# Performance work log

Measured on AMD Instinct MI355X. Metric: run time of the kernel, lower is better.

## Reference

```python
import jax, jax.numpy as jnp
import numpy as np

MAX_SPAN_WIDTH = 30
NUM_WORDS = 2048
NUM_CAND = 8192
HIDDEN = 768
FEAT = 20
FFNN = 1000
SPAN_DIM = HIDDEN * 3 + FEAT  # 2324
TOP_SPAN_NUM = int(NUM_WORDS * 0.4)  # 819


def setup_inputs() -> dict:
    key = jax.random.key(0)
    ks = jax.random.split(key, 16)
    mention_doc = jax.random.normal(ks[0], (NUM_WORDS, HIDDEN), jnp.float32)
    starts = jax.random.randint(ks[1], (NUM_CAND,), 0, NUM_WORDS - MAX_SPAN_WIDTH, jnp.int32)
    widths = jax.random.randint(ks[2], (NUM_CAND,), 1, MAX_SPAN_WIDTH + 1, jnp.int32)
    ends = jnp.minimum(starts + widths - 1, NUM_WORDS - 1).astype(jnp.int32)
    s = 0.02
    lin = lambda k, i, o: jax.random.normal(k, (i, o), jnp.float32) * s
    return dict(
        mention_doc=mention_doc,
        span_width_emb=jax.random.normal(ks[3], (MAX_SPAN_WIDTH, FEAT), jnp.float32) * s,
        head_w=jax.random.normal(ks[4], (HIDDEN,), jnp.float32) * s,
        head_b=jnp.zeros((), jnp.float32),
        m_w1=lin(ks[5], SPAN_DIM, FFNN), m_b1=jnp.zeros((FFNN,), jnp.float32),
        m_w2=lin(ks[6], FFNN, FFNN), m_b2=jnp.zeros((FFNN,), jnp.float32),
        m_w3=jax.random.normal(ks[7], (FFNN,), jnp.float32) * s, m_b3=jnp.zeros((), jnp.float32),
        width_prior_emb=jax.random.normal(ks[8], (MAX_SPAN_WIDTH, FEAT), jnp.float32) * s,
        w_w1=lin(ks[9], FEAT, FFNN), w_b1=jnp.zeros((FFNN,), jnp.float32),
        w_w2=lin(ks[10], FFNN, FFNN), w_b2=jnp.zeros((FFNN,), jnp.float32),
        w_w3=jax.random.normal(ks[11], (FFNN,), jnp.float32) * s, w_b3=jnp.zeros((), jnp.float32),
        candidate_starts=starts,
        candidate_ends=ends,
        top_span_num=TOP_SPAN_NUM,
    )


def get_span_emb(mention_doc, starts, ends, span_width_emb, head_w, head_b):
    # mention_doc: [N, H]; starts/ends: [C]
    num_words = mention_doc.shape[0]
    start_emb = mention_doc[starts]              # [C, H]
    end_emb = mention_doc[ends]                  # [C, H]
    width_ids = ends - starts                    # span width - 1, in [0, MAX_SPAN_WIDTH)
    width_emb = span_width_emb[width_ids]        # [C, F]
    offs = jnp.arange(MAX_SPAN_WIDTH, dtype=starts.dtype)
    idxes = jnp.minimum(starts[:, None] + offs[None, :], num_words - 1)  # [C, W]
    emb_spans = mention_doc[idxes]               # [C, W, H]  (dominant intermediate)
    head_scores = mention_doc @ head_w + head_b  # [N]
    hs = head_scores[idxes]                      # [C, W]
    mask = offs[None, :] <= width_ids[:, None]
    hs = jnp.where(mask, hs, -jnp.inf)
    attn = jax.nn.softmax(hs, axis=1)            # masked softmax over span positions
    attended = jnp.einsum('cw,cwh->ch', attn, emb_spans)
    return jnp.concatenate([start_emb, end_emb, width_emb, attended], axis=-1)  # [C, 3H+F]


def ffnn3(x, w1, b1, w2, b2, w3, b3):
    h = jax.nn.relu(x @ w1 + b1)
    h = jax.nn.relu(h @ w2 + b2)
    return h @ w3 + b3  # [..., ] scalar score per row (Squeezer)


def extract_top_spans(span_scores, starts, ends, top_span_num, num_words):
    # Greedy crossing-interval NMS, faithful to the original sequential algorithm.
    C = span_scores.shape[0]
    order = jnp.argsort(-span_scores)
    offs = jnp.arange(MAX_SPAN_WIDTH, dtype=jnp.int32)

    def body(i, state):
        max_end, min_start, sel, count = state
        idx = order[i]
        s = starts[idx]
        e = ends[idx]
        dup = max_end[s] == e
        j_raw = s + offs
        j = jnp.minimum(j_raw, num_words - 1)
        in_span = j_raw <= e
        # crossing: an already-selected span starting at j>s ends beyond e,
        # or one ending at j<e starts before s.
        c1 = in_span & (j_raw > s) & (max_end[j] > e)
        c2 = in_span & (j_raw < e) & (min_start[j] < s)
        crossed = jnp.any(c1 | c2)
        accept = (~dup) & (~crossed) & (count < top_span_num)
        sel = jnp.where(accept, sel.at[count].set(idx.astype(jnp.int32)), sel)
        max_end = jnp.where(accept, max_end.at[s].max(e), max_end)
        min_start = jnp.where(accept, min_start.at[e].min(s), min_start)
        count = count + accept.astype(jnp.int32)
        return (max_end, min_start, sel, count)

    max_end0 = jnp.full((num_words,), -1, jnp.int32)          # 'not set' sentinel
    min_start0 = jnp.full((num_words,), num_words, jnp.int32)  # 'not set' sentinel
    sel0 = jnp.zeros((top_span_num,), jnp.int32)
    _, _, sel, count = jax.lax.fori_loop(0, C, body, (max_end0, min_start0, sel0, jnp.int32(0)))

    # sort selected spans by (start, end); pad unfilled slots with the first sorted span
    valid = jnp.arange(top_span_num) < count
    keys = jnp.where(valid, starts[sel] * num_words + ends[sel], jnp.iinfo(jnp.int32).max)
    sorted_sel = sel[jnp.argsort(keys)]
    return jnp.where(valid, sorted_sel, sorted_sel[0])


def reference(mention_doc, span_width_emb, head_w, head_b,
              m_w1, m_b1, m_w2, m_b2, m_w3, m_b3,
              width_prior_emb, w_w1, w_b1, w_w2, w_b2, w_w3, w_b3,
              candidate_starts, candidate_ends, top_span_num):
    num_words = mention_doc.shape[0]
    span_emb = get_span_emb(mention_doc, candidate_starts, candidate_ends,
                            span_width_emb, head_w, head_b)            # [C, 2324]
    mention_scores = ffnn3(span_emb, m_w1, m_b1, m_w2, m_b2, m_w3, m_b3)  # [C]
    width_scores = ffnn3(width_prior_emb, w_w1, w_b1, w_w2, w_b2, w_w3, w_b3)  # [30]
    cand_mention_scores = mention_scores + width_scores[candidate_ends - candidate_starts]
    top_idx = extract_top_spans(cand_mention_scores, candidate_starts, candidate_ends,
                                top_span_num, num_words)               # [top]
    top_starts = candidate_starts[top_idx]
    top_ends = candidate_ends[top_idx]
    top_span_emb = span_emb[top_idx]
    top_scores = cand_mention_scores[top_idx]
    return (cand_mention_scores, top_idx, top_starts, top_ends, top_span_emb, top_scores)
```

## Files before the change

kernel.cpp:

```cpp
#include <hip/hip_runtime.h>
#include <cstdio>
#include <cmath>

#define NUM_WORDS 2048
#define NUM_CAND 8192
#define HIDDEN 768
#define FEAT 20
#define FFNN_DIM 1000
#define SPAN_DIM 2324
#define TOP_NUM 819
#define MSW 30
#define KP2 1024
#define NP 1024
#define PNP 3072

#define OUT_TOPIDX   (NUM_CAND)
#define OUT_TSTART   (NUM_CAND + TOP_NUM)
#define OUT_TEND     (NUM_CAND + 2*TOP_NUM)
#define OUT_TEMB     (NUM_CAND + 3*TOP_NUM)
#define OUT_TSCORE   (NUM_CAND + 3*TOP_NUM + TOP_NUM*SPAN_DIM)

typedef short short8 __attribute__((ext_vector_type(8)));
typedef float f32x4 __attribute__((ext_vector_type(4)));
typedef unsigned short u16x4 __attribute__((ext_vector_type(4)));

__device__ __forceinline__ unsigned short bf16_rne(float x) {
    unsigned int u = __float_as_uint(x);
    unsigned int r = u + 0x7FFFu + ((u >> 16) & 1u);
    return (unsigned short)(r >> 16);
}
__device__ __forceinline__ float bf16_to_f(unsigned short h) {
    return __uint_as_float(((unsigned int)h) << 16);
}
__device__ __forceinline__ void store_split3(unsigned short* p0, unsigned short* p1,
                                             unsigned short* p2, size_t off, float v) {
    unsigned short h0 = bf16_rne(v);
    float r1 = v - bf16_to_f(h0);
    unsigned short h1 = bf16_rne(r1);
    float r2 = r1 - bf16_to_f(h1);
    p0[off] = h0;
    p1[off] = h1;
    p2[off] = bf16_rne(r2);
}

__device__ __forceinline__ void gl_lds16(const unsigned short* g, unsigned short* l) {
    __builtin_amdgcn_global_load_lds(
        (const __attribute__((address_space(1))) unsigned short*)g,
        (__attribute__((address_space(3))) unsigned short*)l, 16, 0, 0);
}

__global__ void head_kernel(const float* __restrict__ doc, const float* __restrict__ hw,
                            const float* __restrict__ hb, float* __restrict__ out) {
    int wave = threadIdx.x >> 6, lane = threadIdx.x & 63;
    int row = blockIdx.x * 4 + wave;
    if (row >= NUM_WORDS) return;
    float acc = 0.f;
    for (int h = lane; h < HIDDEN; h += 64) acc += doc[row * HIDDEN + h] * hw[h];
    for (int off = 32; off > 0; off >>= 1) acc += __shfl_down(acc, off);
    if (lane == 0) out[row] = acc + hb[0];
}

__global__ void width_kernel(const float* __restrict__ x, const float* __restrict__ w1,
                             const float* __restrict__ b1, const float* __restrict__ w2,
                             const float* __restrict__ b2, const float* __restrict__ w3,
                             const float* __restrict__ b3, float* __restrict__ out) {
    __shared__ float xs[FEAT];
    __shared__ float h1s[FFNN_DIM];
    __shared__ float red[256];
    int r = blockIdx.x, t = threadIdx.x;
    if (t < FEAT) xs[t] = x[r * FEAT + t];
    __syncthreads();
    for (int j = t; j < FFNN_DIM; j += 256) {
        float acc = b1[j];
        for (int k = 0; k < FEAT; ++k) acc += xs[k] * w1[k * FFNN_DIM + j];
        h1s[j] = fmaxf(acc, 0.f);
    }
    __syncthreads();
    float partial = 0.f;
    for (int j = t; j < FFNN_DIM; j += 256) {
        float acc = b2[j];
        for (int k = 0; k < FFNN_DIM; ++k) acc += h1s[k] * w2[k * FFNN_DIM + j];
        partial += fmaxf(acc, 0.f) * w3[j];
    }
    red[t] = partial;
    __syncthreads();
    for (int s = 128; s > 0; s >>= 1) { if (t < s) red[t] += red[t + s]; __syncthreads(); }
    if (t == 0) out[r] = red[0] + b3[0];
}

__global__ void attn_kernel(const float* __restrict__ head_s, const int* __restrict__ starts,
                            const int* __restrict__ ends, float* __restrict__ attn_g) {
    int wave = threadIdx.x >> 6, w = threadIdx.x & 63;
    int c = blockIdx.x * 4 + wave;
    if (c >= NUM_CAND) return;
    int s = starts[c], e = ends[c];
    int wid = e - s;
    float hsv = -INFINITY;
    if (w < MSW && w <= wid) hsv = head_s[s + w];
    float m = hsv;
    for (int off = 32; off > 0; off >>= 1) m = fmaxf(m, __shfl_down(m, off));
    m = __shfl(m, 0);
    float ex = (w < MSW && w <= wid) ? expf(hsv - m) : 0.f;
    float ssum = ex;
    for (int off = 32; off > 0; off >>= 1) ssum += __shfl_down(ssum, off);
    ssum = __shfl(ssum, 0);
    if (w < 32) attn_g[c * 32 + w] = (w < MSW) ? (ex / ssum) : 0.f;
}

__global__ void doc_convert(const float* __restrict__ doc, unsigned short* __restrict__ d0,
                            unsigned short* __restrict__ d1, unsigned short* __restrict__ d2) {
    int i = blockIdx.x * 256 + threadIdx.x;
    if (i < NUM_WORDS * HIDDEN) store_split3(d0, d1, d2, i, doc[i]);
}

__global__ void convert_wt(const float* __restrict__ w, int K, int N, int Kp,
                           unsigned short* __restrict__ q0, unsigned short* __restrict__ q1,
                           unsigned short* __restrict__ q2) {
    int n = blockIdx.y;
    int k = blockIdx.x * blockDim.x + threadIdx.x;
    if (k >= Kp) return;
    float v = (k < K && n < N) ? w[(size_t)k * N + n] : 0.f;
    store_split3(q0, q1, q2, (size_t)n * Kp + k, v);
}

__global__ void tw_kernel(const float* __restrict__ swe, const float* __restrict__ w1,
                          float* __restrict__ tw) {
    int wid = blockIdx.x, t = threadIdx.x;
    for (int n = t; n < NP; n += 256) {
        float acc = 0.f;
        if (n < FFNN_DIM) {
            for (int f = 0; f < FEAT; ++f)
                acc += swe[wid * FEAT + f] * w1[(size_t)(1536 + f) * FFNN_DIM + n];
        }
        tw[wid * NP + n] = acc;
    }
}

__device__ __forceinline__ void stage_tile(const unsigned short* __restrict__ src,
                                           unsigned short* lds, int base_row, int Kp, int k0,
                                           int t) {
#pragma unroll
    for (int qi = 0; qi < 2; ++qi) {
        int u = qi * 256 + t;
        int l = u & 63;
        int row = ((u >> 6) << 4) + (l >> 2);
        int cblk = (l & 3) ^ (row & 3);
        const unsigned short* g = src + (size_t)(base_row + row) * Kp + k0 + cblk * 8;
        gl_lds16(g, lds + u * 8);
    }
}

__global__ __launch_bounds__(256, 2) void gemm6p(
    const unsigned short* __restrict__ A0, const unsigned short* __restrict__ A1,
    const unsigned short* __restrict__ A2,
    const unsigned short* __restrict__ B0, const unsigned short* __restrict__ B1,
    const unsigned short* __restrict__ B2,
    float* __restrict__ C) {
    __shared__ unsigned short As0[128 * 32], As1[128 * 32], As2[128 * 32];
    __shared__ unsigned short Bs0[128 * 32], Bs1[128 * 32], Bs2[128 * 32];
    int t = threadIdx.x;
    int bid = blockIdx.x;
    int bm = (bid & 15) << 7;
    int bn = (bid >> 4) << 7;
    int lane = t & 63, wv = t >> 6;
    int wm = (wv >> 1) * 64, wn = (wv & 1) * 64;
    int lr = lane & 15, qq = lane >> 4;
    int sw = (qq ^ (lr & 3)) * 8;

    f32x4 acc[4][4] = {};

    for (int k0 = 0; k0 < HIDDEN; k0 += 32) {
        stage_tile(A0, As0, bm, HIDDEN, k0, t);
        stage_tile(A1, As1, bm, HIDDEN, k0, t);
        stage_tile(A2, As2, bm, HIDDEN, k0, t);
        stage_tile(B0, Bs0, bn, HIDDEN, k0, t);
        stage_tile(B1, Bs1, bn, HIDDEN, k0, t);
        stage_tile(B2, Bs2, bn, HIDDEN, k0, t);
        __syncthreads();
        short8 a0[4], a1[4], a2[4];
#pragma unroll
        for (int i = 0; i < 4; ++i) {
            int ra = (wm + i * 16 + lr) * 32 + sw;
            a0[i] = *(const short8*)&As0[ra];
            a1[i] = *(const short8*)&As1[ra];
            a2[i] = *(const short8*)&As2[ra];
        }
#pragma unroll
        for (int j = 0; j < 4; ++j) {
            int rb = (wn + j * 16 + lr) * 32 + sw;
            short8 b0 = *(const short8*)&Bs0[rb];
            short8 b1 = *(const short8*)&Bs1[rb];
            short8 b2 = *(const short8*)&Bs2[rb];
#pragma unroll
            for (int i = 0; i < 4; ++i) {
                acc[i][j] = __builtin_amdgcn_mfma_f32_16x16x32_bf16(a2[i], b0, acc[i][j], 0, 0, 0);
                acc[i][j] = __builtin_amdgcn_mfma_f32_16x16x32_bf16(a0[i], b2, acc[i][j], 0, 0, 0);
                acc[i][j] = __builtin_amdgcn_mfma_f32_16x16x32_bf16(a1[i], b1, acc[i][j], 0, 0, 0);
                acc[i][j] = __builtin_amdgcn_mfma_f32_16x16x32_bf16(a1[i], b0, acc[i][j], 0, 0, 0);
                acc[i][j] = __builtin_amdgcn_mfma_f32_16x16x32_bf16(a0[i], b1, acc[i][j], 0, 0, 0);
                acc[i][j] = __builtin_amdgcn_mfma_f32_16x16x32_bf16(a0[i], b0, acc[i][j], 0, 0, 0);
            }
        }
        __syncthreads();
    }
#pragma unroll
    for (int i = 0; i < 4; ++i)
#pragma unroll
        for (int j = 0; j < 4; ++j)
#pragma unroll
            for (int r = 0; r < 4; ++r) {
                int m = bm + wm + i * 16 + qq * 4 + r;
                int n = bn + wn + j * 16 + lr;
                C[(size_t)m * PNP + n] = acc[i][j][r];
            }
}

__global__ void combine_kernel(const float* __restrict__ P, const float* __restrict__ tw,
                               const float* __restrict__ attn_g, const float* __restrict__ b1,
                               const int* __restrict__ starts, const int* __restrict__ ends,
                               unsigned short* __restrict__ h0, unsigned short* __restrict__ h1,
                               unsigned short* __restrict__ h2) {
    int c = blockIdx.x, t = threadIdx.x;
    int s = starts[c], e = ends[c];
    int wid = e - s;
    __shared__ float at[MSW];
    if (t < MSW) at[t] = attn_g[c * 32 + t];
    __syncthreads();
    int n0 = t * 4;
    size_t ho = (size_t)c * NP + n0;
    if (t < 250) {
        f32x4 acc = *(const f32x4*)&P[(size_t)s * PNP + n0];
        acc += *(const f32x4*)&P[(size_t)e * PNP + 1024 + n0];
        acc += *(const f32x4*)&tw[(size_t)wid * NP + n0];
        acc += *(const f32x4*)&b1[n0];
        const float* Pa = P + (size_t)s * PNP + 2048 + n0;
        for (int w = 0; w <= wid; ++w)
            acc += at[w] * *(const f32x4*)&Pa[(size_t)w * PNP];
        u16x4 q0, q1, q2;
#pragma unroll
        for (int k = 0; k < 4; ++k) {
            float v = fmaxf(acc[k], 0.f);
            unsigned short x0 = bf16_rne(v);
            float r1 = v - bf16_to_f(x0);
            unsigned short x1 = bf16_rne(r1);
            float r2 = r1 - bf16_to_f(x1);
            q0[k] = x0; q1[k] = x1; q2[k] = bf16_rne(r2);
        }
        *(u16x4*)&h0[ho] = q0;
        *(u16x4*)&h1[ho] = q1;
        *(u16x4*)&h2[ho] = q2;
    } else {
        u16x4 z = {0, 0, 0, 0};
        *(u16x4*)&h0[ho] = z;
        *(u16x4*)&h1[ho] = z;
        *(u16x4*)&h2[ho] = z;
    }
}

__global__ __launch_bounds__(256, 2) void gemm6(
    const unsigned short* __restrict__ A0, const unsigned short* __restrict__ A1,
    const unsigned short* __restrict__ A2,
    const unsigned short* __restrict__ B0, const unsigned short* __restrict__ B1,
    const unsigned short* __restrict__ B2,
    const float* __restrict__ bias, int nreal, int Kp,
    const float* __restrict__ w3, float* __restrict__ partials) {
    __shared__ unsigned short As0[128 * 32], As1[128 * 32], As2[128 * 32];
    __shared__ unsigned short Bs0[128 * 32], Bs1[128 * 32], Bs2[128 * 32];
    int t = threadIdx.x;
    int bid = blockIdx.x;
    int sm = bid >> 6, idx = bid & 63;
    int bm = ((sm << 3) + (idx & 7)) << 7;
    int bn = (idx >> 3) << 7;
    int lane = t & 63, wv = t >> 6;
    int wm = (wv >> 1) * 64, wn = (wv & 1) * 64;
    int lr = lane & 15, qq = lane >> 4;
    int sw = (qq ^ (lr & 3)) * 8;

    f32x4 acc[4][4] = {};

    for (int k0 = 0; k0 < Kp; k0 += 32) {
        stage_tile(A0, As0, bm, Kp, k0, t);
        stage_tile(A1, As1, bm, Kp, k0, t);
        stage_tile(A2, As2, bm, Kp, k0, t);
        stage_tile(B0, Bs0, bn, Kp, k0, t);
        stage_tile(B1, Bs1, bn, Kp, k0, t);
        stage_tile(B2, Bs2, bn, Kp, k0, t);
        __syncthreads();
        short8 a0[4], a1[4], a2[4];
#pragma unroll
        for (int i = 0; i < 4; ++i) {
            int ra = (wm + i * 16 + lr) * 32 + sw;
            a0[i] = *(const short8*)&As0[ra];
            a1[i] = *(const short8*)&As1[ra];
            a2[i] = *(const short8*)&As2[ra];
        }
#pragma unroll
        for (int j = 0; j < 4; ++j) {
            int rb = (wn + j * 16 + lr) * 32 + sw;
            short8 b0 = *(const short8*)&Bs0[rb];
            short8 b1 = *(const short8*)&Bs1[rb];
            short8 b2 = *(const short8*)&Bs2[rb];
#pragma unroll
            for (int i = 0; i < 4; ++i) {
                acc[i][j] = __builtin_amdgcn_mfma_f32_16x16x32_bf16(a2[i], b0, acc[i][j], 0, 0, 0);
                acc[i][j] = __builtin_amdgcn_mfma_f32_16x16x32_bf16(a0[i], b2, acc[i][j], 0, 0, 0);
                acc[i][j] = __builtin_amdgcn_mfma_f32_16x16x32_bf16(a1[i], b1, acc[i][j], 0, 0, 0);
                acc[i][j] = __builtin_amdgcn_mfma_f32_16x16x32_bf16(a1[i], b0, acc[i][j], 0, 0, 0);
                acc[i][j] = __builtin_amdgcn_mfma_f32_16x16x32_bf16(a0[i], b1, acc[i][j], 0, 0, 0);
                acc[i][j] = __builtin_amdgcn_mfma_f32_16x16x32_bf16(a0[i], b0, acc[i][j], 0, 0, 0);
            }
        }
        __syncthreads();
    }

    int pid = ((bn >> 7) << 1) | (wn >> 6);
#pragma unroll
    for (int i = 0; i < 4; ++i)
#pragma unroll
        for (int r = 0; r < 4; ++r) {
            float p = 0.f;
#pragma unroll
            for (int j = 0; j < 4; ++j) {
                int n = bn + wn + j * 16 + lr;
                float v = acc[i][j][r] + (n < nreal ? bias[n] : 0.f);
                v = fmaxf(v, 0.f);
                p += v * (n < nreal ? w3[n] : 0.f);
            }
            p += __shfl_xor(p, 1);
            p += __shfl_xor(p, 2);
            p += __shfl_xor(p, 4);
            p += __shfl_xor(p, 8);
            if (lr == 0) {
                int m = bm + wm + i * 16 + qq * 4 + r;
                partials[(size_t)m * 16 + pid] = p;
            }
        }
}

__global__ void score_final(const float* __restrict__ partials, const float* __restrict__ b3,
                            const float* __restrict__ width_s, const int* __restrict__ starts,
                            const int* __restrict__ ends, float* __restrict__ out) {
    int c = blockIdx.x * 256 + threadIdx.x;
    if (c >= NUM_CAND) return;
    float s = b3[0] + width_s[ends[c] - starts[c]];
#pragma unroll
    for (int p = 0; p < 16; ++p) s += partials[(size_t)c * 16 + p];
    out[c] = s;
}

__global__ __launch_bounds__(256) void rank_kernel(const float* __restrict__ scores,
                                                   const int* __restrict__ starts,
                                                   const int* __restrict__ ends,
                                                   unsigned short* __restrict__ ord_g,
                                                   unsigned int* __restrict__ se_g) {
    __shared__ unsigned long long kk[NUM_CAND];
    int t = threadIdx.x;
    for (int i = t; i < NUM_CAND; i += 256) {
        unsigned int b = __float_as_uint(scores[i]);
        unsigned int u = b ^ ((b & 0x80000000u) ? 0xFFFFFFFFu : 0x80000000u);
        unsigned int hi = ~u;
        kk[i] = ((unsigned long long)hi << 32) | (unsigned int)i;
    }
    __syncthreads();
    int c = blockIdx.x * 32 + (t >> 3);
    int seg = (t & 7) * 1024;
    unsigned long long mykey = kk[c];
    int cnt = 0;
    for (int i = seg; i < seg + 1024; ++i) cnt += (kk[i] < mykey) ? 1 : 0;
    cnt += __shfl_xor(cnt, 1);
    cnt += __shfl_xor(cnt, 2);
    cnt += __shfl_xor(cnt, 4);
    if ((t & 7) == 0) {
        int idx = (int)(mykey & 0xFFFFFFFFull);
        int rank = cnt;
        ord_g[rank] = (unsigned short)idx;
        se_g[rank] = ((unsigned int)starts[idx] << 16) | (unsigned int)ends[idx];
    }
}

__global__ __launch_bounds__(64, 1)
void select_nms(const unsigned int* __restrict__ se_g,
                unsigned short* __restrict__ sel_g,
                int* __restrict__ count_g) {
    __shared__ unsigned int se_arr[NUM_CAND];
    __shared__ unsigned int st[2 * NUM_WORDS];
    int lane = threadIdx.x;

    {
        const uint4* src4 = (const uint4*)se_g;
        uint4* dst4 = (uint4*)se_arr;
        for (int i = lane; i < NUM_CAND / 4; i += 64) dst4[i] = src4[i];
    }
    for (int i = lane; i < 2 * NUM_WORDS; i += 64)
        st[i] = (i & 1) ? (unsigned int)NUM_WORDS : 0u;
    __syncthreads();

    const unsigned long long* stp = (const unsigned long long*)st;
    int count = 0;
    for (int c = 0; c < NUM_CAND / 64; ++c) {
        int ib = c * 64;
        unsigned int sev = se_arr[ib + lane];
        int s = (int)(sev >> 16), e = (int)(sev & 0xFFFFu);
        const unsigned long long* bp = stp + s;
        unsigned long long v[MSW];
#pragma unroll
        for (int w = 0; w < MSW; ++w) v[w] = bp[w];
        int me = (int)(unsigned int)v[0] - 1;
        bool crossedA = (s < e) && ((int)(unsigned int)(v[0] >> 32) < s);
        bool crossedB = false;
#pragma unroll
        for (int w = 1; w < MSW; ++w) {
            int j = s + w;
            bool in = (j <= e);
            int mej = (int)(unsigned int)v[w] - 1;
            int msj = (int)(unsigned int)(v[w] >> 32);
            bool hit = in && ((mej > e) || ((j < e) && (msj < s)));
            if (w & 1) crossedA = crossedA || hit;
            else       crossedB = crossedB || hit;
        }
        bool crossed = crossedA || crossedB;
        bool spec = !crossed && (me != e);

        int cbefore = count;
        unsigned long long window = ~0ull;
        unsigned int pend = 0u;
        int rk = 0, lcnt = 0;
        while (true) {
            unsigned long long b = __ballot(spec) & window;
            if (b == 0ull) break;
            int f = __ffsll((unsigned long long)b) - 1;
            unsigned int sef = __builtin_amdgcn_readlane(sev, (unsigned int)f);
            int sf = (int)(sef >> 16), ef = (int)(sef & 0xFFFFu);
            bool mine = (lane == lcnt);
            pend = mine ? sef : pend;
            rk = mine ? (ib + f) : rk;
            lcnt++;
            count++;
            if (count >= TOP_NUM) break;
            window &= (f >= 63) ? 0ull : (~0ull << (f + 1));
            if (lane > f) {
                if (s == sf) me = max(me, ef);
                crossed = crossed || ((s < sf) && (sf <= e) && (ef > e))
                                  || ((sf < s) && (s <= ef) && (ef < e));
                spec = !crossed && (me != e);
            }
        }
        if (lane < lcnt) {
            int sf = (int)(pend >> 16), ef = (int)(pend & 0xFFFFu);
            sel_g[cbefore + lane] = (unsigned short)rk;
            atomicMax(&st[2 * sf], (unsigned int)(ef + 1));
            atomicMin(&st[2 * ef + 1], (unsigned int)sf);
        }
        if (count >= TOP_NUM) break;
    }
    if (lane == 0) *count_g = count;
}

__global__ __launch_bounds__(256) void select_post(const float* __restrict__ scores,
                                                   const int* __restrict__ starts,
                                                   const int* __restrict__ ends,
                                                   const unsigned short* __restrict__ ord_g,
                                                   const unsigned short* __restrict__ sel_g,
                                                   const int* __restrict__ count_g,
                                                   float* out, int* top_idx_ws) {
    __shared__ unsigned long long fkeys[1024];
    int t = threadIdx.x;
    int count = *count_g;
    for (int i = t; i < 1024; i += 256) {
        unsigned long long k = 0xFFFFFFFFFFFFFFFFull;
        if (i < count) {
            int idx = (int)ord_g[sel_g[i]];
            unsigned int key32 = (unsigned int)(starts[idx] * NUM_WORDS + ends[idx]);
            k = ((unsigned long long)key32 << 32) | (unsigned int)idx;
        }
        fkeys[i] = k;
    }
    __syncthreads();
    for (int size = 2; size <= 1024; size <<= 1) {
        for (int stride = size >> 1; stride > 0; stride >>= 1) {
            for (int i = t; i < 1024; i += 256) {
                int ixj = i ^ stride;
                if (ixj > i) {
                    bool up = ((i & size) == 0);
                    unsigned long long a = fkeys[i], b = fkeys[ixj];
                    if ((a > b) == up) { fkeys[i] = b; fkeys[ixj] = a; }
                }
            }
            __syncthreads();
        }
    }
    for (int i = t; i < TOP_NUM; i += 256) {
        int fi = (i < count) ? (int)(fkeys[i] & 0xFFFFFFFFull)
                             : (int)(fkeys[0] & 0xFFFFFFFFull);
        out[OUT_TOPIDX + i] = (float)fi;
        out[OUT_TSTART + i] = (float)starts[fi];
        out[OUT_TEND + i] = (float)ends[fi];
        out[OUT_TSCORE + i] = scores[fi];
        top_idx_ws[i] = fi;
    }
}

__global__ void gather_emb(const float* __restrict__ doc, const float* __restrict__ swe,
                           const float* __restrict__ attn_g, const int* __restrict__ starts,
                           const int* __restrict__ ends, const int* __restrict__ top_idx_ws,
                           float* __restrict__ out) {
    int r = blockIdx.x, t = threadIdx.x;
    int idx = top_idx_ws[r];
    int s = starts[idx], e = ends[idx];
    int wid = e - s;
    __shared__ float at[MSW];
    if (t < MSW) at[t] = attn_g[(size_t)idx * 32 + t];
    __syncthreads();
    float* dst = out + OUT_TEMB + (size_t)r * SPAN_DIM;
    if (t < 192) {
        int h4 = t * 4;
        f32x4 vs = *(const f32x4*)&doc[(size_t)s * HIDDEN + h4];
        f32x4 ve = *(const f32x4*)&doc[(size_t)e * HIDDEN + h4];
        f32x4 acc = {0.f, 0.f, 0.f, 0.f};
        for (int w = 0; w <= wid; ++w)
            acc += at[w] * *(const f32x4*)&doc[(size_t)(s + w) * HIDDEN + h4];
#pragma unroll
        for (int k = 0; k < 4; ++k) {
            dst[h4 + k] = vs[k];
            dst[HIDDEN + h4 + k] = ve[k];
            dst[2 * HIDDEN + FEAT + h4 + k] = acc[k];
        }
    }
    if (t < FEAT) dst[2 * HIDDEN + t] = swe[wid * FEAT + t];
}

extern "C" void kernel_launch(void* const* d_in, const int* in_sizes, int n_in,
                              void* d_out, int out_size, void* d_ws, size_t ws_size,
                              hipStream_t stream) {
    const float* mention_doc = (const float*)d_in[0];
    const float* span_width_emb = (const float*)d_in[1];
    const float* head_w = (const float*)d_in[2];
    const float* head_b = (const float*)d_in[3];
    const float* m_w1 = (const float*)d_in[4];
    const float* m_b1 = (const float*)d_in[5];
    const float* m_w2 = (const float*)d_in[6];
    const float* m_b2 = (const float*)d_in[7];
    const float* m_w3 = (const float*)d_in[8];
    const float* m_b3 = (const float*)d_in[9];
    const float* width_prior_emb = (const float*)d_in[10];
    const float* w_w1 = (const float*)d_in[11];
    const float* w_b1 = (const float*)d_in[12];
    const float* w_w2 = (const float*)d_in[13];
    const float* w_b2 = (const float*)d_in[14];
    const float* w_w3 = (const float*)d_in[15];
    const float* w_b3 = (const float*)d_in[16];
    const int* cand_starts = (const int*)d_in[17];
    const int* cand_ends = (const int*)d_in[18];

    char* w = (char*)d_ws;
    const size_t szH = (size_t)NUM_CAND * NP * 2;
    const size_t szW2 = (size_t)NP * KP2 * 2;
    const size_t szWc = (size_t)PNP * HIDDEN * 2;
    const size_t szD = (size_t)NUM_WORDS * HIDDEN * 2;
    char* p = w;
    unsigned short* h0 = (unsigned short*)p; p += szH;
    unsigned short* h1 = (unsigned short*)p; p += szH;
    unsigned short* h2 = (unsigned short*)p; p += szH;
    unsigned short* w2t0 = (unsigned short*)p; p += szW2;
    unsigned short* w2t1 = (unsigned short*)p; p += szW2;
    unsigned short* w2t2 = (unsigned short*)p; p += szW2;
    unsigned short* Wc0 = (unsigned short*)p; p += szWc;
    unsigned short* Wc1 = (unsigned short*)p; p += szWc;
    unsigned short* Wc2 = (unsigned short*)p; p += szWc;
    unsigned short* d0 = (unsigned short*)p; p += szD;
    unsigned short* d1 = (unsigned short*)p; p += szD;
    unsigned short* d2 = (unsigned short*)p; p += szD;
    float* P = (float*)p; p += (size_t)NUM_WORDS * PNP * 4;
    float* tw = (float*)p; p += (size_t)MSW * NP * 4;
    float* attn_g = (float*)p; p += (size_t)NUM_CAND * 32 * 4;
    float* partials = (float*)p; p += (size_t)NUM_CAND * 16 * 4;
    unsigned short* ord_g = (unsigned short*)p; p += (size_t)NUM_CAND * 2;
    unsigned int* se_g = (unsigned int*)p; p += (size_t)NUM_CAND * 4;
    unsigned short* sel_g = (unsigned short*)p; p += 2048;
    int* count_g = (int*)p; p += 128;
    float* head_s = (float*)p; p += NUM_WORDS * 4;
    float* width_s = (float*)p; p += 128;
    int* top_idx_ws = (int*)p; p += 4096;

    size_t need = (size_t)(p - w);
    if (ws_size < need) {
        fprintf(stderr, "kernel_launch: ws too small (%zu < %zu)\n", ws_size, need);
    }

    float* out = (float*)d_out;

    head_kernel<<<NUM_WORDS / 4, 256, 0, stream>>>(mention_doc, head_w, head_b, head_s);
    width_kernel<<<MSW, 256, 0, stream>>>(width_prior_emb, w_w1, w_b1, w_w2, w_b2, w_w3, w_b3,
                                          width_s);
    attn_kernel<<<NUM_CAND / 4, 256, 0, stream>>>(head_s, cand_starts, cand_ends, attn_g);
    doc_convert<<<(NUM_WORDS * HIDDEN + 255) / 256, 256, 0, stream>>>(mention_doc, d0, d1, d2);
    convert_wt<<<dim3(3, 1024), 256, 0, stream>>>(m_w1, HIDDEN, FFNN_DIM, HIDDEN,
                                                  Wc0, Wc1, Wc2);
    convert_wt<<<dim3(3, 1024), 256, 0, stream>>>(m_w1 + (size_t)HIDDEN * FFNN_DIM, HIDDEN,
                                                  FFNN_DIM, HIDDEN,
                                                  Wc0 + (size_t)1024 * HIDDEN,
                                                  Wc1 + (size_t)1024 * HIDDEN,
                                                  Wc2 + (size_t)1024 * HIDDEN);
    convert_wt<<<dim3(3, 1024), 256, 0, stream>>>(m_w1 + (size_t)1556 * FFNN_DIM, HIDDEN,
                                                  FFNN_DIM, HIDDEN,
                                                  Wc0 + (size_t)2048 * HIDDEN,
                                                  Wc1 + (size_t)2048 * HIDDEN,
                                                  Wc2 + (size_t)2048 * HIDDEN);
    convert_wt<<<dim3(4, 1024), 256, 0, stream>>>(m_w2, FFNN_DIM, FFNN_DIM, KP2,
                                                  w2t0, w2t1, w2t2);
    tw_kernel<<<MSW, 256, 0, stream>>>(span_width_emb, m_w1, tw);
    gemm6p<<<16 * 24, 256, 0, stream>>>(d0, d1, d2, Wc0, Wc1, Wc2, P);
    combine_kernel<<<NUM_CAND, 256, 0, stream>>>(P, tw, attn_g, m_b1, cand_starts, cand_ends,
                                                 h0, h1, h2);
    gemm6<<<512, 256, 0, stream>>>(h0, h1, h2, w2t0, w2t1, w2t2, m_b2, FFNN_DIM, KP2,
                                   m_w3, partials);
    score_final<<<NUM_CAND / 256, 256, 0, stream>>>(partials, m_b3, width_s, cand_starts,
                                                    cand_ends, out);
    rank_kernel<<<NUM_CAND / 32, 256, 0, stream>>>(out, cand_starts, cand_ends, ord_g, se_g);
    select_nms<<<1, 64, 0, stream>>>(se_g, sel_g, count_g);
    select_post<<<1, 256, 0, stream>>>(out, cand_starts, cand_ends, ord_g, sel_g, count_g,
                                       out, top_idx_ws);
    gather_emb<<<TOP_NUM, 256, 0, stream>>>(mention_doc, span_width_emb, attn_g, cand_starts,
                                            cand_ends, top_idx_ws, out);
}
```

Measured before the change: 869.7 us.

## Prefetch next NMS chunk's state in select_nms and merge weight conversion launches

The serial single-wave NMS loop now loads the next 64 candidates' span table entries and evaluates their crossing checks while the current chunk is resolved. It then patches those results using the spans just selected, read back with readlane, which hides LDS load latency on the critical serial path. Separately, the three convert_wt launches for the m_w1 segments are replaced by one convert_wc launch covering all three. The risk is extra register pressure from the 30-entry prefetch array and a per-lane fix-up loop over newly selected spans.

```diff
diff --git a/kernel.cpp b/kernel.cpp
--- a/kernel.cpp
+++ b/kernel.cpp
@@ -121,6 +121,18 @@
     if (k >= Kp) return;
     float v = (k < K && n < N) ? w[(size_t)k * N + n] : 0.f;
     store_split3(q0, q1, q2, (size_t)n * Kp + k, v);
+}
+
+__global__ void convert_wc(const float* __restrict__ w1,
+                           unsigned short* __restrict__ q0, unsigned short* __restrict__ q1,
+                           unsigned short* __restrict__ q2) {
+    int n2 = blockIdx.y;
+    int seg = n2 >> 10;
+    int n = n2 & 1023;
+    int k = blockIdx.x * 256 + threadIdx.x;
+    int row0 = (seg == 0) ? 0 : ((seg == 1) ? HIDDEN : 1556);
+    float v = (n < FFNN_DIM) ? w1[(size_t)(row0 + k) * FFNN_DIM + n] : 0.f;
+    store_split3(q0, q1, q2, (size_t)n2 * HIDDEN + k, v);
 }
 
 __global__ void tw_kernel(const float* __restrict__ swe, const float* __restrict__ w1,
@@ -396,18 +408,19 @@
     __syncthreads();
 
     const unsigned long long* stp = (const unsigned long long*)st;
-    int count = 0;
-    for (int c = 0; c < NUM_CAND / 64; ++c) {
-        int ib = c * 64;
-        unsigned int sev = se_arr[ib + lane];
-        int s = (int)(sev >> 16), e = (int)(sev & 0xFFFFu);
+
+    unsigned int sev = se_arr[lane];
+    int s = (int)(sev >> 16), e = (int)(sev & 0xFFFFu);
+    int me;
+    bool crossed;
+    {
         const unsigned long long* bp = stp + s;
         unsigned long long v[MSW];
 #pragma unroll
         for (int w = 0; w < MSW; ++w) v[w] = bp[w];
-        int me = (int)(unsigned int)v[0] - 1;
-        bool crossedA = (s < e) && ((int)(unsigned int)(v[0] >> 32) < s);
-        bool crossedB = false;
+        me = (int)(unsigned int)v[0] - 1;
+        bool cA = (s < e) && ((int)(unsigned int)(v[0] >> 32) < s);
+        bool cB = false;
 #pragma unroll
         for (int w = 1; w < MSW; ++w) {
             int j = s + w;
@@ -415,11 +428,27 @@
             int mej = (int)(unsigned int)v[w] - 1;
             int msj = (int)(unsigned int)(v[w] >> 32);
             bool hit = in && ((mej > e) || ((j < e) && (msj < s)));
-            if (w & 1) crossedA = crossedA || hit;
-            else       crossedB = crossedB || hit;
-        }
-        bool crossed = crossedA || crossedB;
-        bool spec = !crossed && (me != e);
+            if (w & 1) cA = cA || hit; else cB = cB || hit;
+        }
+        crossed = cA || cB;
+    }
+    bool spec = !crossed && (me != e);
+
+    int count = 0;
+    for (int c = 0; c < NUM_CAND / 64; ++c) {
+        int ib = c * 64;
+        bool have_next = (c + 1 < NUM_CAND / 64);
+        unsigned int sev_n = 0;
+        int s_n = 0, e_n = 0;
+        unsigned long long vn[MSW];
+        if (have_next) {
+            sev_n = se_arr[ib + 64 + lane];
+            s_n = (int)(sev_n >> 16);
+            e_n = (int)(sev_n & 0xFFFFu);
+            const unsigned long long* bp = stp + s_n;
+#pragma unroll
+            for (int w = 0; w < MSW; ++w) vn[w] = bp[w];
+        }
 
         int cbefore = count;
         unsigned long long window = ~0ull;
@@ -451,7 +480,30 @@
             atomicMax(&st[2 * sf], (unsigned int)(ef + 1));
             atomicMin(&st[2 * ef + 1], (unsigned int)sf);
         }
-        if (count >= TOP_NUM) break;
+        if (count >= TOP_NUM || !have_next) break;
+
+        int me_n = (int)(unsigned int)vn[0] - 1;
+        bool cA = (s_n < e_n) && ((int)(unsigned int)(vn[0] >> 32) < s_n);
+        bool cB = false;
+#pragma unroll
+        for (int w = 1; w < MSW; ++w) {
+            int j = s_n + w;
+            bool in = (j <= e_n);
+            int mej = (int)(unsigned int)vn[w] - 1;
+            int msj = (int)(unsigned int)(vn[w] >> 32);
+            bool hit = in && ((mej > e_n) || ((j < e_n) && (msj < s_n)));
+            if (w & 1) cA = cA || hit; else cB = cB || hit;
+        }
+        bool crossed_n = cA || cB;
+        for (int k = 0; k < lcnt; ++k) {
+            unsigned int sef = __builtin_amdgcn_readlane(pend, (unsigned int)k);
+            int sf = (int)(sef >> 16), ef = (int)(sef & 0xFFFFu);
+            if (s_n == sf) me_n = max(me_n, ef);
+            crossed_n = crossed_n || ((s_n < sf) && (sf <= e_n) && (ef > e_n))
+                                  || ((sf < s_n) && (s_n <= ef) && (ef < e_n));
+        }
+        sev = sev_n; s = s_n; e = e_n; me = me_n; crossed = crossed_n;
+        spec = !crossed && (me != e);
     }
     if (lane == 0) *count_g = count;
 }
@@ -594,18 +646,7 @@
                                           width_s);
     attn_kernel<<<NUM_CAND / 4, 256, 0, stream>>>(head_s, cand_starts, cand_ends, attn_g);
     doc_convert<<<(NUM_WORDS * HIDDEN + 255) / 256, 256, 0, stream>>>(mention_doc, d0, d1, d2);
-    convert_wt<<<dim3(3, 1024), 256, 0, stream>>>(m_w1, HIDDEN, FFNN_DIM, HIDDEN,
-                                                  Wc0, Wc1, Wc2);
-    convert_wt<<<dim3(3, 1024), 256, 0, stream>>>(m_w1 + (size_t)HIDDEN * FFNN_DIM, HIDDEN,
-                                                  FFNN_DIM, HIDDEN,
-                                                  Wc0 + (size_t)1024 * HIDDEN,
-                                                  Wc1 + (size_t)1024 * HIDDEN,
-                                                  Wc2 + (size_t)1024 * HIDDEN);
-    convert_wt<<<dim3(3, 1024), 256, 0, stream>>>(m_w1 + (size_t)1556 * FFNN_DIM, HIDDEN,
-                                                  FFNN_DIM, HIDDEN,
-                                                  Wc0 + (size_t)2048 * HIDDEN,
-                                                  Wc1 + (size_t)2048 * HIDDEN,
-                                                  Wc2 + (size_t)2048 * HIDDEN);
+    convert_wc<<<dim3(3, 3072), 256, 0, stream>>>(m_w1, Wc0, Wc1, Wc2);
     convert_wt<<<dim3(4, 1024), 256, 0, stream>>>(m_w2, FFNN_DIM, FFNN_DIM, KP2,
                                                   w2t0, w2t1, w2t2);
     tw_kernel<<<MSW, 256, 0, stream>>>(span_width_emb, m_w1, tw);
```

Result: slower. 944.8 us (+8.6%).

## Resolve NMS chunk dependencies in parallel waves and merge w1 conversion launches

Applied to the files above, without the earlier changes.

The single-wave NMS selection no longer accepts one candidate per ballot iteration. It first builds, for each lane, a mask of earlier lanes in the 64-candidate chunk that could affect it. It then decides every lane whose dependencies are resolved in the same round, so a chunk needs roughly as many ballots as the longest dependency chain rather than one per accepted span. Separately, the three convert_wt launches for m_w1 segments are fused into a single convert_wc launch. The serial select_nms kernel is on the critical path, so this targets latency, at the cost of a pre-pass over earlier lanes per chunk and more complex logic that must reproduce the greedy ordering exactly.

```diff
diff --git a/kernel.cpp b/kernel.cpp
--- a/kernel.cpp
+++ b/kernel.cpp
@@ -121,6 +121,18 @@
     if (k >= Kp) return;
     float v = (k < K && n < N) ? w[(size_t)k * N + n] : 0.f;
     store_split3(q0, q1, q2, (size_t)n * Kp + k, v);
+}
+
+__global__ void convert_wc(const float* __restrict__ w1,
+                           unsigned short* __restrict__ q0, unsigned short* __restrict__ q1,
+                           unsigned short* __restrict__ q2) {
+    int n2 = blockIdx.y;
+    int seg = n2 >> 10;
+    int n = n2 & 1023;
+    int k = blockIdx.x * 256 + threadIdx.x;
+    int row0 = (seg == 0) ? 0 : ((seg == 1) ? HIDDEN : 1556);
+    float v = (n < FFNN_DIM) ? w1[(size_t)(row0 + k) * FFNN_DIM + n] : 0.f;
+    store_split3(q0, q1, q2, (size_t)n2 * HIDDEN + k, v);
 }
 
 __global__ void tw_kernel(const float* __restrict__ swe, const float* __restrict__ w1,
@@ -396,6 +408,7 @@
     __syncthreads();
 
     const unsigned long long* stp = (const unsigned long long*)st;
+    unsigned long long lane_below = (lane == 0) ? 0ull : (~0ull >> (64 - lane));
     int count = 0;
     for (int c = 0; c < NUM_CAND / 64; ++c) {
         int ib = c * 64;
@@ -419,38 +432,57 @@
             else       crossedB = crossedB || hit;
         }
         bool crossed = crossedA || crossedB;
-        bool spec = !crossed && (me != e);
-
-        int cbefore = count;
-        unsigned long long window = ~0ull;
-        unsigned int pend = 0u;
-        int rk = 0, lcnt = 0;
-        while (true) {
-            unsigned long long b = __ballot(spec) & window;
-            if (b == 0ull) break;
-            int f = __ffsll((unsigned long long)b) - 1;
-            unsigned int sef = __builtin_amdgcn_readlane(sev, (unsigned int)f);
+        bool undec = !crossed;
+
+        unsigned long long undec_mask = __ballot(undec);
+        unsigned long long pb = 0ull;
+        unsigned long long mm = undec_mask & lane_below;
+        while (mm) {
+            int b = __ffsll((unsigned long long)mm) - 1;
+            mm &= mm - 1;
+            unsigned int sef = __builtin_amdgcn_readlane(sev, (unsigned int)b);
             int sf = (int)(sef >> 16), ef = (int)(sef & 0xFFFFu);
-            bool mine = (lane == lcnt);
-            pend = mine ? sef : pend;
-            rk = mine ? (ib + f) : rk;
-            lcnt++;
-            count++;
-            if (count >= TOP_NUM) break;
-            window &= (f >= 63) ? 0ull : (~0ull << (f + 1));
-            if (lane > f) {
-                if (s == sf) me = max(me, ef);
-                crossed = crossed || ((s < sf) && (sf <= e) && (ef > e))
-                                  || ((sf < s) && (s <= ef) && (ef < e));
-                spec = !crossed && (me != e);
+            bool rel = (sf == s)
+                    || ((s < sf) && (sf <= e) && (ef > e))
+                    || ((sf < s) && (s <= ef) && (ef < e));
+            if (rel) pb |= (1ull << b);
+        }
+
+        unsigned long long undecided = undec_mask;
+        unsigned long long accm = 0ull;
+        while (undecided) {
+            bool ready = undec && ((pb & undecided) == 0ull);
+            unsigned long long dec = __ballot(ready);
+            bool spec = !crossed && (me != e);
+            unsigned long long newacc = __ballot(ready && spec);
+            unsigned long long m2 = newacc;
+            while (m2) {
+                int b = __ffsll((unsigned long long)m2) - 1;
+                m2 &= m2 - 1;
+                unsigned int sef = __builtin_amdgcn_readlane(sev, (unsigned int)b);
+                int sf = (int)(sef >> 16), ef = (int)(sef & 0xFFFFu);
+                if (lane > b) {
+                    if (s == sf) me = max(me, ef);
+                    crossed = crossed || ((s < sf) && (sf <= e) && (ef > e))
+                                      || ((sf < s) && (s <= ef) && (ef < e));
+                }
             }
-        }
-        if (lane < lcnt) {
-            int sf = (int)(pend >> 16), ef = (int)(pend & 0xFFFFu);
-            sel_g[cbefore + lane] = (unsigned short)rk;
-            atomicMax(&st[2 * sf], (unsigned int)(ef + 1));
-            atomicMin(&st[2 * ef + 1], (unsigned int)sf);
-        }
+            undec = undec && !ready;
+            undecided &= ~dec;
+            accm |= newacc;
+        }
+
+        int navail = TOP_NUM - count;
+        int nacc = __popcll(accm);
+        int ntake = (nacc < navail) ? nacc : navail;
+        bool acc_l = ((accm >> lane) & 1ull) != 0ull;
+        int myord = __popcll(accm & lane_below);
+        if (acc_l && myord < ntake) {
+            sel_g[count + myord] = (unsigned short)(ib + lane);
+            atomicMax(&st[2 * s], (unsigned int)(e + 1));
+            atomicMin(&st[2 * e + 1], (unsigned int)s);
+        }
+        count += ntake;
         if (count >= TOP_NUM) break;
     }
     if (lane == 0) *count_g = count;
@@ -594,18 +626,7 @@
                                           width_s);
     attn_kernel<<<NUM_CAND / 4, 256, 0, stream>>>(head_s, cand_starts, cand_ends, attn_g);
     doc_convert<<<(NUM_WORDS * HIDDEN + 255) / 256, 256, 0, stream>>>(mention_doc, d0, d1, d2);
-    convert_wt<<<dim3(3, 1024), 256, 0, stream>>>(m_w1, HIDDEN, FFNN_DIM, HIDDEN,
-                                                  Wc0, Wc1, Wc2);
-    convert_wt<<<dim3(3, 1024), 256, 0, stream>>>(m_w1 + (size_t)HIDDEN * FFNN_DIM, HIDDEN,
-                                                  FFNN_DIM, HIDDEN,
-                                                  Wc0 + (size_t)1024 * HIDDEN,
-                                                  Wc1 + (size_t)1024 * HIDDEN,
-                                                  Wc2 + (size_t)1024 * HIDDEN);
-    convert_wt<<<dim3(3, 1024), 256, 0, stream>>>(m_w1 + (size_t)1556 * FFNN_DIM, HIDDEN,
-                                                  FFNN_DIM, HIDDEN,
-                                                  Wc0 + (size_t)2048 * HIDDEN,
-                                                  Wc1 + (size_t)2048 * HIDDEN,
-                                                  Wc2 + (size_t)2048 * HIDDEN);
+    convert_wc<<<dim3(3, 3072), 256, 0, stream>>>(m_w1, Wc0, Wc1, Wc2);
     convert_wt<<<dim3(4, 1024), 256, 0, stream>>>(m_w2, FFNN_DIM, FFNN_DIM, KP2,
                                                   w2t0, w2t1, w2t2);
     tw_kernel<<<MSW, 256, 0, stream>>>(span_width_emb, m_w1, tw);
```

Result: slower. 920.0 us (+5.8%).
